# Performance work log

Measured on AMD Instinct MI355X. Metric: run time of the kernel, lower is better.

## Reference

```python
import jax, jax.numpy as jnp
import numpy as np

# ---- static dims ----
B, L, V = 8, 512, 100000
E, NERD, COREFD = 100, 20, 20          # word / ner / coref embedding dims
H, DIS, REL, HT = 128, 20, 97, 512     # hidden, dis embed, relations, n_pairs
W, N, R, C = 512, 32, 8, 256           # DNC word len, cells, read heads, ctrl hidden
IN_SIZE = E + NERD + COREFD            # 140 == H + 12 (required by final_layer)
DNC_OUT = H + 12                        # 140
CTRL_IN = IN_SIZE + R * W               # 4236
MASK_MIN, EPS, CLIP = 0.1, 1e-6, 20.0
# interface vector layout: read keys, read strengths, write key, write strength,
# erase, write vec, free gates, alloc gate, write gate, read modes,
# write mask, read masks, fwd sharpness, bwd sharpness
XI_SIZES = [R*W, R, W, 1, W, W, R, 1, 1, 3*R, W, R*W, R, R]
XI = sum(XI_SIZES)


def setup_inputs():
    key = jax.random.key(0)
    ks = iter(jax.random.split(key, 40))
    def nrm(shape, s=0.02):
        return (jax.random.normal(next(ks), shape) * s).astype(jnp.float32)
    def ri(shape, hi):
        return jax.random.randint(next(ks), shape, 0, hi)
    return dict(
        context_idxs=ri((B, L), V),
        pos=ri((B, L), L),
        context_ner=ri((B, L), 7),
        context_char_idxs=ri((B, L, 16), 262),
        context_lens=jnp.full((B,), L, dtype=jnp.int32),
        h_mapping=jax.random.uniform(next(ks), (B, HT, L), jnp.float32) / L,
        t_mapping=jax.random.uniform(next(ks), (B, HT, L), jnp.float32) / L,
        relation_mask=jnp.ones((B, HT), jnp.float32),
        dis_h_2_t=ri((B, HT), 20),
        dis_t_2_h=ri((B, HT), 20),
        word_emb=nrm((V, E), 0.1),
        entity_emb=nrm((L, COREFD), 0.1),
        ner_emb=nrm((7, NERD), 0.1),
        dis_emb=nrm((20, DIS), 0.1),
        Wih0=nrm((CTRL_IN, 4*C)), Whh0=nrm((C, 4*C)), b0=jnp.zeros((4*C,), jnp.float32),
        Wih1=nrm((C, 4*C)), Whh1=nrm((C, 4*C)), b1=jnp.zeros((4*C,), jnp.float32),
        Wih2=nrm((C, 4*C)), Whh2=nrm((C, 4*C)), b2=jnp.zeros((4*C,), jnp.float32),
        W_xi=nrm((C, XI)), b_xi=jnp.zeros((XI,), jnp.float32),
        W_out=nrm((C + R*W, DNC_OUT)), b_out=jnp.zeros((DNC_OUT,), jnp.float32),
        W_final=nrm((DNC_OUT, 2*H)), b_final=jnp.zeros((2*H,), jnp.float32),
        W_re=nrm((2*H, H)), b_re=jnp.zeros((H,), jnp.float32),
        W_bili=nrm((REL, H+DIS, H+DIS)), b_bili=jnp.zeros((REL,), jnp.float32),
    )


def _lstm(x, h, c, Wih, Whh, b):
    z = x @ Wih + h @ Whh + b
    i, f, g, o = jnp.split(z, 4, axis=-1)
    c = jax.nn.sigmoid(f) * c + jax.nn.sigmoid(i) * jnp.tanh(g)
    h = jax.nn.sigmoid(o) * jnp.tanh(c)
    return h, c


def _content(M, key_, beta, mask):
    # M [B,N,W]; key_, mask [B,h,W]; beta [B,h] -> weights [B,h,N]
    k = key_ * mask
    Mm = M[:, None] * mask[:, :, None]                 # [B,h,N,W]
    dot = jnp.einsum('bhw,bhnw->bhn', k, Mm)
    kn = jnp.linalg.norm(k, axis=-1)[..., None]
    Mn = jnp.linalg.norm(Mm, axis=-1)
    cos = dot / (kn * Mn + EPS)
    return jax.nn.softmax(beta[..., None] * cos, axis=-1)


def _sharpen(w, s):
    w = (w + EPS) ** s[..., None]
    return w / w.sum(-1, keepdims=True)


def _dnc(x, params):
    (Wih0, Whh0, b0, Wih1, Whh1, b1, Wih2, Whh2, b2, W_xi, b_xi, W_out, b_out) = params
    Bs = x.shape[0]
    eye = jnp.eye(N, dtype=x.dtype)
    splits = np.cumsum(XI_SIZES)[:-1]

    def step(carry, x_t):
        (h0, c0, h1, c1, h2, c2, M, u, wr, ww, p, Lnk, reads) = carry
        ci = jnp.concatenate([x_t, reads.reshape(Bs, R*W)], -1)
        h0, c0 = _lstm(ci, h0, c0, Wih0, Whh0, b0)
        h1, c1 = _lstm(h0, h1, c1, Wih1, Whh1, b1)
        h2, c2 = _lstm(h1, h2, c2, Wih2, Whh2, b2)
        h = jnp.clip(h2, -CLIP, CLIP)
        xi = h @ W_xi + b_xi
        (rk, rb, wk, wb, er, wv, fg, ga, gw, rm,
         wmask, rmask, sf, sb) = jnp.split(xi, splits, axis=-1)
        rk = rk.reshape(Bs, R, W)
        rb = 1 + jax.nn.softplus(rb)                    # [B,R]
        wk = wk.reshape(Bs, 1, W)
        wb = 1 + jax.nn.softplus(wb)                    # [B,1]
        er = jax.nn.sigmoid(er)                         # [B,W]
        fg = jax.nn.sigmoid(fg)                         # [B,R]
        ga = jax.nn.sigmoid(ga)
        gw = jax.nn.sigmoid(gw)
        pi = jax.nn.softmax(rm.reshape(Bs, R, 3), -1)
        wmask = MASK_MIN + (1 - MASK_MIN) * jax.nn.sigmoid(wmask)
        rmask = MASK_MIN + (1 - MASK_MIN) * jax.nn.sigmoid(rmask).reshape(Bs, R, W)
        sf = 1 + jax.nn.softplus(sf)
        sb = 1 + jax.nn.softplus(sb)

        # retention / usage
        psi = jnp.prod(1 - fg[:, :, None] * wr, axis=1)  # [B,N]
        u = (u + ww - u * ww) * psi
        # allocation weighting via sorted free list
        order = jnp.argsort(u, axis=-1)
        us = jnp.take_along_axis(u, order, -1)
        cp = jnp.cumprod(jnp.concatenate([jnp.ones((Bs, 1), u.dtype), us[:, :-1]], -1), -1)
        a_s = (1 - us) * cp
        a = jnp.zeros_like(u).at[jnp.arange(Bs)[:, None], order].set(a_s)
        # write addressing (masked content + allocation)
        cw = _content(M, wk, wb, wmask[:, None, :])[:, 0]
        ww = gw * (ga * a + (1 - ga) * cw)
        # de-allocate content of freed cells, then write
        M = M * psi[:, :, None]
        M = M * (1 - ww[:, :, None] * er[:, None, :]) + ww[:, :, None] * wv[:, None, :]
        # temporal link matrix (uses previous precedence p)
        Lnk = (1 - ww[:, :, None] - ww[:, None, :]) * Lnk + ww[:, :, None] * p[:, None, :]
        Lnk = Lnk * (1 - eye)
        p = (1 - ww.sum(-1, keepdims=True)) * p + ww
        # read addressing with link sharpness control
        fw = _sharpen(jnp.einsum('bij,brj->bri', Lnk, wr), sf)
        bw = _sharpen(jnp.einsum('bji,brj->bri', Lnk, wr), sb)
        cr = _content(M, rk, rb, rmask)
        wr = pi[..., 0:1] * bw + pi[..., 1:2] * cr + pi[..., 2:3] * fw
        reads = jnp.einsum('brn,bnw->brw', wr, M)
        y = jnp.concatenate([h, reads.reshape(Bs, R*W)], -1) @ W_out + b_out
        return (h0, c0, h1, c1, h2, c2, M, u, wr, ww, p, Lnk, reads), y

    z = jnp.zeros
    carry0 = (z((Bs, C)), z((Bs, C)), z((Bs, C)), z((Bs, C)), z((Bs, C)), z((Bs, C)),
              z((Bs, N, W)), z((Bs, N)), z((Bs, R, N)), z((Bs, N)), z((Bs, N)),
              z((Bs, N, N)), z((Bs, R, W)))
    _, ys = jax.lax.scan(step, carry0, x.transpose(1, 0, 2))
    return ys.transpose(1, 0, 2)  # [B,L,DNC_OUT]


def reference(context_idxs, pos, context_ner, context_char_idxs, context_lens,
              h_mapping, t_mapping, relation_mask, dis_h_2_t, dis_t_2_h,
              word_emb, entity_emb, ner_emb, dis_emb,
              Wih0, Whh0, b0, Wih1, Whh1, b1, Wih2, Whh2, b2,
              W_xi, b_xi, W_out, b_out, W_final, b_final, W_re, b_re,
              W_bili, b_bili):
    sent = jnp.concatenate([word_emb[context_idxs], entity_emb[pos],
                            ner_emb[context_ner]], -1)      # [B,L,140]
    dnc_params = (Wih0, Whh0, b0, Wih1, Whh1, b1, Wih2, Whh2, b2,
                  W_xi, b_xi, W_out, b_out)
    out = _dnc(sent, dnc_params)                             # [B,L,140]
    out = out @ W_final + b_final                            # LockedDropout: identity (eval)
    ctx = jax.nn.relu(out @ W_re + b_re)                     # [B,L,H]
    s0 = jnp.einsum('bpl,blh->bph', h_mapping, ctx)
    t0 = jnp.einsum('bpl,blh->bph', t_mapping, ctx)
    s_rep = jnp.concatenate([s0, dis_emb[dis_h_2_t]], -1)    # [B,P,148]
    t_rep = jnp.concatenate([t0, dis_emb[dis_t_2_h]], -1)
    return jnp.einsum('bpi,kij,bpj->bpk', s_rep, W_bili, t_rep) + b_bili
```

## Files before the change

### kernel.cpp

```cpp
#include <hip/hip_runtime.h>
#include <math.h>

#define B8      8
#define LSEQ    512
#define NWG     256
#define TPB     512
#define RELK    97
#define BI      148
#define FSTR    16
#define LDSF    39040
#define LDSB    (LDSF*4)

__device__ __forceinline__ float sigf(float x){
  return (x >= 0.f) ? 1.f/(1.f + expf(-x)) : expf(x)/(1.f + expf(x));
}
__device__ __forceinline__ float spf(float x){
  return (x > 0.f) ? x + log1pf(expf(-x)) : log1pf(expf(x));
}

__device__ __forceinline__ float agld(const float* p){
  return __hip_atomic_load(p, __ATOMIC_RELAXED, __HIP_MEMORY_SCOPE_AGENT);
}
__device__ __forceinline__ void agst(float* p, float v){
  __hip_atomic_store(p, v, __ATOMIC_RELAXED, __HIP_MEMORY_SCOPE_AGENT);
}

__global__ __launch_bounds__(256)
void k_sent(const int* __restrict__ cidx, const int* __restrict__ pos,
            const int* __restrict__ ner, const float* __restrict__ wemb,
            const float* __restrict__ eemb, const float* __restrict__ nemb,
            float* __restrict__ sent)
{
  int flat = blockIdx.x*256 + threadIdx.x;
  if (flat >= B8*LSEQ*140) return;
  int d = flat % 140; int bl = flat / 140;
  float v;
  if (d < 100)      v = wemb[(size_t)cidx[bl]*100 + d];
  else if (d < 120) v = eemb[(size_t)pos[bl]*20 + (d-100)];
  else              v = nemb[(size_t)ner[bl]*20 + (d-120)];
  sent[flat] = v;
}

__global__ __launch_bounds__(256)
void k_tr(const float* __restrict__ A, const float* __restrict__ Bsrc,
          int N, int K1a, int K1b, int K2, long long total, float* __restrict__ T)
{
  long long i = (long long)blockIdx.x*256 + threadIdx.x;
  if (i >= total) return;
  int k = (int)(i % K2);
  long long c = i / K2;
  float v = 0.f;
  if (k < K1a)            v = A[(size_t)k*N + c];
  else if (k < K1a+K1b)   v = Bsrc[(size_t)(k-K1a)*N + c];
  T[i] = v;
}

__device__ __forceinline__ void gbar(int* flags, int* genrep, int seq){
  __syncthreads();
  const int tid = threadIdx.x;
  const int bid = blockIdx.x;
  if (tid == 0){
    asm volatile("s_waitcnt vmcnt(0)" ::: "memory");
    __hip_atomic_store(&flags[bid*FSTR], seq, __ATOMIC_RELAXED, __HIP_MEMORY_SCOPE_AGENT);
  }
  if (bid == 0){
    if (tid < NWG){
      while (__hip_atomic_load(&flags[tid*FSTR], __ATOMIC_RELAXED, __HIP_MEMORY_SCOPE_AGENT) < seq)
        __builtin_amdgcn_s_sleep(2);
    }
    __syncthreads();
    if (tid < 32)
      __hip_atomic_store(&genrep[tid*FSTR], seq, __ATOMIC_RELAXED, __HIP_MEMORY_SCOPE_AGENT);
  } else if (tid == 0){
    while (__hip_atomic_load(&genrep[(bid & 31)*FSTR], __ATOMIC_RELAXED, __HIP_MEMORY_SCOPE_AGENT) < seq)
      __builtin_amdgcn_s_sleep(2);
  }
  __syncthreads();
}

__device__ void mem_phase(float* lds, const float* __restrict__ xi,
                          float* __restrict__ M, float* u_g, float* ww_g,
                          float* p_g, float* wr_g, float* L_g, float* rout)
{
  const int tid = threadIdx.x;
  float* mL  = lds;
  float* mwr = lds+1024;
  float* mwrn= lds+1280;
  float* mcr = lds+1536;
  float* mfw = lds+1792;
  float* mbw = lds+2048;
  float* PSI = lds+2304;
  float* UU  = lds+2336;
  float* US  = lds+2368;
  float* AA  = lds+2400;
  float* CW  = lds+2432;
  float* WWN = lds+2464;
  float* WWO = lds+2496;
  float* PP  = lds+2528;
  int*   mord= (int*)(lds+2560);
  float* mh  = lds+2592;
  float* mpi = lds+2656;
  float* msc = lds+2688;
  float* q1  = lds+2752;
  float* q2  = lds+3264;

  if (tid < 8){
    mh[tid]    = 1.f + spf(agld(&xi[4096+tid]));
    mh[8+tid]  = 1.f + spf(agld(&xi[10283+tid]));
    mh[16+tid] = 1.f + spf(agld(&xi[10291+tid]));
    mh[24+tid] = sigf(agld(&xi[5641+tid]));
    float e0=agld(&xi[5651+3*tid]), e1=agld(&xi[5652+3*tid]), e2=agld(&xi[5653+3*tid]);
    float mx=fmaxf(e0,fmaxf(e1,e2));
    float x0=expf(e0-mx), x1=expf(e1-mx), x2=expf(e2-mx);
    float inv=1.f/(x0+x1+x2);
    mpi[tid*3]=x0*inv; mpi[tid*3+1]=x1*inv; mpi[tid*3+2]=x2*inv;
  }
  if (tid==0){ msc[0]=1.f+spf(agld(&xi[4616])); msc[1]=sigf(agld(&xi[5649])); msc[2]=sigf(agld(&xi[5650])); }
  if (tid<32){ UU[tid]=u_g[tid]; WWO[tid]=ww_g[tid]; PP[tid]=p_g[tid]; }
  if (tid<256) mwr[tid]=wr_g[tid];
  mL[tid]=L_g[tid]; mL[tid+512]=L_g[tid+512];
  { float wm = 0.1f+0.9f*sigf(agld(&xi[5675+tid])); q1[tid]=agld(&xi[4104+tid])*wm; q2[tid]=wm; }
  __syncthreads();

  if (tid<32){
    float psi=1.f;
    #pragma unroll
    for (int r=0;r<8;r++) psi *= (1.f - mh[24+r]*mwr[r*32+tid]);
    PSI[tid]=psi;
    float uo=UU[tid], wo=WWO[tid];
    UU[tid]=(uo+wo-uo*wo)*psi;
  }
  __syncthreads();
  if (tid<32){
    float un=UU[tid]; int rank=0;
    for (int m=0;m<32;m++){ float um=UU[m]; rank += (um<un)||(um==un && m<tid); }
    mord[rank]=tid;
  }
// ... 62 lines not shown
    __syncthreads();
    if (tid==0){ float qq=0.f; for(int i=0;i<8;i++) qq+=msc[8+i]; msc[32]=sqrtf(qq); }
    __syncthreads();
    { int n=tid>>4, wsub=tid&15;
      float d=0.f,q=0.f;
      for (int i=0;i<32;i++){ int w=wsub+16*i; float m=M[(size_t)n*512+w]; float t2=m*q2[w]; d+=q1[w]*t2; q+=t2*t2; }
      for (int o=8;o;o>>=1){ d+=__shfl_down(d,o,16); q+=__shfl_down(q,o,16); }
      if (wsub==0){ float cs=d/(msc[32]*sqrtf(q)+1e-6f); mcr[r*32+n]=mh[r]*cs; } }
    __syncthreads();
  }
  if (tid<8){ int r=tid; float mx=-1e30f;
    for (int n=0;n<32;n++) mx=fmaxf(mx,mcr[r*32+n]);
    float sm=0.f;
    for (int n=0;n<32;n++){ float e=expf(mcr[r*32+n]-mx); mcr[r*32+n]=e; sm+=e; }
    float inv=1.f/sm;
    for (int n=0;n<32;n++) mcr[r*32+n]*=inv; }
  __syncthreads();
  if (tid<256){ int r=tid>>5, n=tid&31;
    float v=mpi[r*3]*mbw[r*32+n]+mpi[r*3+1]*mcr[r*32+n]+mpi[r*3+2]*mfw[r*32+n];
    mwrn[tid]=v; wr_g[tid]=v; }
  __syncthreads();
  { int r=tid>>6, wsub=tid&63;
    for (int i2=0;i2<8;i2++){ int w=wsub+64*i2;
      float accv=0.f;
      for (int n=0;n<32;n++) accv+=mwrn[r*32+n]*M[(size_t)n*512+w];
      agst(&rout[r*512+w], accv); } }
  if (tid<32){ u_g[tid]=UU[tid]; ww_g[tid]=WWN[tid]; p_g[tid]=PP[tid]; }
  L_g[tid]=mL[tid]; L_g[tid+512]=mL[tid+512];
}

__global__ __launch_bounds__(TPB, 1)
void dnc_persist(
  const float* __restrict__ sent,
  const float* __restrict__ WAg, const float* __restrict__ b0,
  const float* __restrict__ W1g, const float* __restrict__ b1,
  const float* __restrict__ W2g, const float* __restrict__ b2,
  const float* __restrict__ WXIg,const float* __restrict__ bxi,
  const float* __restrict__ WY,  const float* __restrict__ bout,
  float* __restrict__ Hh, float* __restrict__ yh,
  float* __restrict__ reads2,
  float* __restrict__ h0g, float* __restrict__ h1g, float* __restrict__ h2g,
  float* __restrict__ c0g, float* __restrict__ c1g, float* __restrict__ c2g,
  float* __restrict__ z0g, float* __restrict__ z1g, float* __restrict__ z2g,
  float* __restrict__ xig,
  float* __restrict__ Mb, float* __restrict__ ug, float* __restrict__ wwg,
  float* __restrict__ pg, float* __restrict__ wrg, float* __restrict__ Lg,
  int* flags, int* genrep)
{
  extern __shared__ float lds[];
  float* sA   = lds;
  float* sRed = lds + 4160;
  float* wA   = lds + 4224;
  float* w1l  = lds + 22656;
  float* w2l  = lds + 24704;
  float* wxl  = lds + 26752;
  const int wg  = blockIdx.x;
  const int tid = threadIdx.x;
  const int cq = tid >> 7, kq = tid & 127;
  const int xc = tid >> 6, xk = tid & 63;
  int seq = 0;

  for (int f=tid; f<18432; f+=TPB) wA[f]  = WAg[(size_t)wg*18432 + f];
  for (int f=tid; f<2048;  f+=TPB) w1l[f] = W1g[(size_t)wg*2048  + f];
  for (int f=tid; f<2048;  f+=TPB) w2l[f] = W2g[(size_t)wg*2048  + f];
  for (int f=tid; f<12288; f+=TPB){
    int cl = f>>8, k = f&255; int col = wg*48 + cl;
    wxl[f] = (col < 10299) ? WXIg[(size_t)col*256 + k] : 0.f;
  }
  const bool isy = (wg >= 8 && wg < 148);
  const float* wcolY = WY + (size_t)(isy ? (wg-8) : 0)*4352;
  __syncthreads();

  #pragma unroll 1
  for (int t=0; t<LSEQ; t++){
    const int rp = t&1, wp = rp^1, pprev = (t+1)&1;
    const float* readsPrev = reads2 + (size_t)pprev*32768;

    {
      const float* h0p = h0g + pprev*2048;
      float acc[8] = {0,0,0,0,0,0,0,0};
      float av[8];
      #pragma unroll
      for (int s=0;s<8;s++){
        int kg = tid;
        av[s] = (kg<140) ? sent[((size_t)s*512 + t)*140 + kg]
                         : agld(&readsPrev[s*4096 + kg - 140]);
      }
      #pragma unroll 1
      for (int ch=0; ch<9; ch++){
        __syncthreads();
        #pragma unroll
        for (int s=0;s<8;s++) sA[s*520 + tid] = av[s];
        __syncthreads();
        if (ch < 8){
          int kg = (ch+1)*512 + tid;
          #pragma unroll
          for (int s=0;s<8;s++){
            float v;
            if (kg < 140)       v = sent[((size_t)s*512 + t)*140 + kg];
            else if (kg < 4236) v = agld(&readsPrev[s*4096 + kg - 140]);
            else if (kg < 4492) v = agld(&h0p[s*256 + (kg-4236)]);
            else                v = 0.f;
            av[s]=v;
          }
        }
        float4 wv = *reinterpret_cast<const float4*>(&wA[cq*4608 + ch*512 + (kq<<2)]);
        #pragma unroll
        for (int s=0;s<8;s++){
          float4 a = *reinterpret_cast<const float4*>(&sA[s*520 + (kq<<2)]);
          acc[s] += a.x*wv.x + a.y*wv.y + a.z*wv.z + a.w*wv.w;
        }
      }
      #pragma unroll
      for (int o=32;o;o>>=1)
        #pragma unroll
        for (int s=0;s<8;s++) acc[s]+=__shfl_down(acc[s],o,64);
      if ((tid&63)==0){ int wv2=tid>>6;
        #pragma unroll
        for (int s=0;s<8;s++) sRed[wv2*8+s]=acc[s]; }
      __syncthreads();
      if (tid<32){ int c=tid>>3, s=tid&7;
        agst(&z0g[s*1024 + wg*4 + c], sRed[c*16+s] + sRed[c*16+8+s] + b0[wg*4+c]); }
    }
    gbar(flags,genrep,++seq);

    {
      float4 w1v = *reinterpret_cast<const float4*>(&w1l[cq*512 + (kq<<2)]);
      if (tid<256){
        int j=tid;
        #pragma unroll
        for (int s=0;s<8;s++){
          float zi=agld(&z0g[s*1024+j]), zf=agld(&z0g[s*1024+256+j]);
          float zg=agld(&z0g[s*1024+512+j]), zo=agld(&z0g[s*1024+768+j]);
          float cold=agld(&c0g[rp*2048+s*256+j]);
          float cn=sigf(zf)*cold+sigf(zi)*tanhf(zg);
          float h=sigf(zo)*tanhf(cn);
          sA[s*520+j]=h;
          if (wg==8){ agst(&c0g[wp*2048+s*256+j],cn); agst(&h0g[rp*2048+s*256+j],h); }
        }
      } else {
        int j=tid-256;
        const float* h1p = h1g + pprev*2048;
        #pragma unroll
        for (int s=0;s<8;s++) sA[s*520+256+j]=agld(&h1p[s*256+j]);
      }
      __syncthreads();
      float acc[8]={0,0,0,0,0,0,0,0};
      #pragma unroll
      for (int s=0;s<8;s++){
        float4 a=*reinterpret_cast<const float4*>(&sA[s*520+(kq<<2)]);
        acc[s]+=a.x*w1v.x+a.y*w1v.y+a.z*w1v.z+a.w*w1v.w;
      }
      #pragma unroll
      for (int o=32;o;o>>=1)
        #pragma unroll
        for (int s=0;s<8;s++) acc[s]+=__shfl_down(acc[s],o,64);
      if ((tid&63)==0){ int wv2=tid>>6;
        #pragma unroll
        for (int s=0;s<8;s++) sRed[wv2*8+s]=acc[s]; }
      __syncthreads();
      if (tid<32){ int c=tid>>3, s=tid&7;
        agst(&z1g[s*1024 + wg*4 + c], sRed[c*16+s] + sRed[c*16+8+s] + b1[wg*4+c]); }
    }
    gbar(flags,genrep,++seq);

    {
      float4 w2v = *reinterpret_cast<const float4*>(&w2l[cq*512 + (kq<<2)]);
      if (tid<256){
        int j=tid;
        #pragma unroll
        for (int s=0;s<8;s++){
          float zi=agld(&z1g[s*1024+j]), zf=agld(&z1g[s*1024+256+j]);
          float zg=agld(&z1g[s*1024+512+j]), zo=agld(&z1g[s*1024+768+j]);
          float cold=agld(&c1g[rp*2048+s*256+j]);
          float cn=sigf(zf)*cold+sigf(zi)*tanhf(zg);
          float h=sigf(zo)*tanhf(cn);
          sA[s*520+j]=h;
          if (wg==8){ agst(&c1g[wp*2048+s*256+j],cn); agst(&h1g[rp*2048+s*256+j],h); }
        }
      } else {
        int j=tid-256;
        const float* h2p = h2g + pprev*2048;
        #pragma unroll
        for (int s=0;s<8;s++) sA[s*520+256+j]=agld(&h2p[s*256+j]);
      }
      __syncthreads();
      float acc[8]={0,0,0,0,0,0,0,0};
      #pragma unroll
      for (int s=0;s<8;s++){
        float4 a=*reinterpret_cast<const float4*>(&sA[s*520+(kq<<2)]);
        acc[s]+=a.x*w2v.x+a.y*w2v.y+a.z*w2v.z+a.w*w2v.w;
      }
      #pragma unroll
      for (int o=32;o;o>>=1)
        #pragma unroll
        for (int s=0;s<8;s++) acc[s]+=__shfl_down(acc[s],o,64);
      if ((tid&63)==0){ int wv2=tid>>6;
        #pragma unroll
        for (int s=0;s<8;s++) sRed[wv2*8+s]=acc[s]; }
      __syncthreads();
      if (tid<32){ int c=tid>>3, s=tid&7;
        agst(&z2g[s*1024 + wg*4 + c], sRed[c*16+s] + sRed[c*16+8+s] + b2[wg*4+c]); }
    }
    gbar(flags,genrep,++seq);

    {
      if (tid<256){
        int j=tid;
        #pragma unroll
        for (int s=0;s<8;s++){
          float zi=agld(&z2g[s*1024+j]), zf=agld(&z2g[s*1024+256+j]);
          float zg=agld(&z2g[s*1024+512+j]), zo=agld(&z2g[s*1024+768+j]);
          float cold=agld(&c2g[rp*2048+s*256+j]);
          float cn=sigf(zf)*cold+sigf(zi)*tanhf(zg);
          float h2=sigf(zo)*tanhf(cn);
          float hc=fminf(fmaxf(h2,-20.f),20.f);
          sA[s*520+j]=hc;
          if (wg==8){ agst(&c2g[wp*2048+s*256+j],cn); agst(&h2g[rp*2048+s*256+j],h2);
                      agst(&Hh[((size_t)t*8+s)*256+j],hc); }
        }
      }
      __syncthreads();
      float accx[6][8];
      #pragma unroll
      for (int cc=0;cc<6;cc++)
        #pragma unroll
        for (int s=0;s<8;s++) accx[cc][s]=0.f;
      #pragma unroll
      for (int s=0;s<8;s++){
        float4 a = *reinterpret_cast<const float4*>(&sA[s*520 + (xk<<2)]);
        #pragma unroll
        for (int cc=0;cc<6;cc++){
          float4 wv = *reinterpret_cast<const float4*>(&wxl[(xc*6+cc)*256 + (xk<<2)]);
          accx[cc][s] += a.x*wv.x + a.y*wv.y + a.z*wv.z + a.w*wv.w;
        }
      }
      #pragma unroll
      for (int o=32;o;o>>=1)
        #pragma unroll
        for (int cc=0;cc<6;cc++)
          #pragma unroll
          for (int s=0;s<8;s++) accx[cc][s]+=__shfl_down(accx[cc][s],o,64);
      if ((tid&63)==0){
        #pragma unroll
        for (int cc=0;cc<6;cc++){
          int col = wg*48 + xc*6 + cc;
          if (col < 10299){
            #pragma unroll
            for (int s=0;s<8;s++) agst(&xig[(size_t)s*10299+col], accx[cc][s]+bxi[col]);
          }
        }
      }
    }
    gbar(flags,genrep,++seq);

    if (wg < 8){
      mem_phase(lds, xig + (size_t)wg*10299, Mb + (size_t)wg*16384,
                ug+wg*32, wwg+wg*32, pg+wg*32, wrg+wg*256, Lg+wg*1024,
                reads2 + (size_t)rp*32768 + wg*4096);
    } else if (isy && t > 0){
      int ty = t-1;
      const float* rdp = reads2 + (size_t)(ty&1)*32768;
      float wy[9];
      #pragma unroll
      for (int ch=0;ch<9;ch++){ int k=ch*512+tid; wy[ch]=(k<4352)? wcolY[k] : 0.f; }
      float acy[8]={0,0,0,0,0,0,0,0};
      #pragma unroll
      for (int ch=0;ch<9;ch++){
        int kg=ch*512+tid;
        #pragma unroll
        for (int s=0;s<8;s++){
          float a;
          if (kg<256)       a=agld(&Hh[((size_t)ty*8+s)*256+kg]);
          else if (kg<4352) a=agld(&rdp[s*4096+kg-256]);
          else              a=0.f;
          acy[s]+=a*wy[ch];
        }
      }
      #pragma unroll
      for (int o=32;o;o>>=1)
        #pragma unroll
        for (int s=0;s<8;s++) acy[s]+=__shfl_down(acy[s],o,64);
      if ((tid&63)==0){ int wv2=tid>>6;
        #pragma unroll
        for (int s=0;s<8;s++) sRed[wv2*8+s]=acy[s]; }
      __syncthreads();
      if (tid<8){ float v=0.f;
        #pragma unroll
        for (int w=0;w<8;w++) v+=sRed[w*8+tid];
        yh[((size_t)tid*512+ty)*140+(wg-8)]=v+bout[wg-8]; }
    }
    gbar(flags,genrep,++seq);
  }

  if (isy){
    int ty = 511;
    const float* rdp = reads2 + (size_t)(ty&1)*32768;
    float wy[9];
    #pragma unroll
    for (int ch=0;ch<9;ch++){ int k=ch*512+tid; wy[ch]=(k<4352)? wcolY[k] : 0.f; }
    float acy[8]={0,0,0,0,0,0,0,0};
    #pragma unroll
    for (int ch=0;ch<9;ch++){
      int kg=ch*512+tid;
      #pragma unroll
      for (int s=0;s<8;s++){
        float a;
        if (kg<256)       a=agld(&Hh[((size_t)ty*8+s)*256+kg]);
        else if (kg<4352) a=agld(&rdp[s*4096+kg-256]);
        else              a=0.f;
        acy[s]+=a*wy[ch];
      }
    }
    #pragma unroll
    for (int o=32;o;o>>=1)
      #pragma unroll
      for (int s=0;s<8;s++) acy[s]+=__shfl_down(acy[s],o,64);
    if ((tid&63)==0){ int wv2=tid>>6;
      #pragma unroll
      for (int s=0;s<8;s++) sRed[wv2*8+s]=acy[s]; }
    __syncthreads();
    if (tid<8){ float v=0.f;
      #pragma unroll
      for (int w=0;w<8;w++) v+=sRed[w*8+tid];
      yh[((size_t)tid*512+ty)*140+(wg-8)]=v+bout[wg-8]; }
  }
}

__global__ __launch_bounds__(256)
void gemm16(int M, int N, int K,
            const float* __restrict__ A, long long sAb, int lda,
            const float* __restrict__ Bm, long long sBb, int ldb,
            float* __restrict__ C, long long sCb, int ldc,
            const float* __restrict__ bias, int relu)
{
  __shared__ float sAh[16*512];
  const int tid = threadIdx.x;
  const float* Ab = A + (size_t)blockIdx.y*sAb;
  const float* Bb = Bm + (size_t)blockIdx.y*sBb;
  float* Cb = C + (size_t)blockIdx.y*sCb;
  const int m0 = blockIdx.x*16;
  const int tot = 16*K;
  for (int f = tid; f < tot; f += 256) sAh[f] = Ab[(size_t)m0*lda + f];
  __syncthreads();
  int c = (tid & 63)*4; int rg = tid >> 6;
  if (c >= N) return;
  float acc[4][4] = {};
  for (int k=0;k<K;k++){
    float4 bv = *reinterpret_cast<const float4*>(Bb + (size_t)k*ldb + c);
    #pragma unroll
    for (int rr=0;rr<4;rr++){
      float a = sAh[(rg*4+rr)*K + k];
      acc[rr][0] += a*bv.x; acc[rr][1] += a*bv.y; acc[rr][2] += a*bv.z; acc[rr][3] += a*bv.w;
    }
  }
  for (int rr=0;rr<4;rr++){
    int m = m0 + rg*4 + rr;
    #pragma unroll
// ... 75 lines not shown
  const int*   ctx_idx = (const int*)  d_in[0];
  const int*   pos     = (const int*)  d_in[1];
  const int*   nerI    = (const int*)  d_in[2];
  const float* h_map   = (const float*)d_in[5];
  const float* t_map   = (const float*)d_in[6];
  const int*   dht     = (const int*)  d_in[8];
  const int*   dth     = (const int*)  d_in[9];
  const float* wemb    = (const float*)d_in[10];
  const float* eemb    = (const float*)d_in[11];
  const float* nemb    = (const float*)d_in[12];
  const float* demb    = (const float*)d_in[13];
  const float* Wih0    = (const float*)d_in[14];
  const float* Whh0    = (const float*)d_in[15];
  const float* b0      = (const float*)d_in[16];
  const float* Wih1    = (const float*)d_in[17];
  const float* Whh1    = (const float*)d_in[18];
  const float* b1      = (const float*)d_in[19];
  const float* Wih2    = (const float*)d_in[20];
  const float* Whh2    = (const float*)d_in[21];
  const float* b2      = (const float*)d_in[22];
  const float* Wxi     = (const float*)d_in[23];
  const float* bxi     = (const float*)d_in[24];
  const float* Wout    = (const float*)d_in[25];
  const float* bout    = (const float*)d_in[26];
  const float* Wfin    = (const float*)d_in[27];
  const float* bfin    = (const float*)d_in[28];
  const float* Wre     = (const float*)d_in[29];
  const float* bre     = (const float*)d_in[30];
  const float* Wbili   = (const float*)d_in[31];
  const float* bbili   = (const float*)d_in[32];

  float* ws    = (float*)d_ws;
  float* sent  = ws;
  float* Hh    = sent + 573440;
  float* yh    = Hh + 1048576;
  float* s0b   = yh + 573440;
  float* t0b   = s0b + 524288;
  float* reads2= t0b + 524288;
  float* h0g   = reads2 + 65536;
  float* h1g   = h0g + 4096;
  float* h2g   = h1g + 4096;
  float* c0g   = h2g + 4096;
  float* c1g   = c0g + 4096;
  float* c2g   = c1g + 4096;
  float* z0g   = c2g + 4096;
  float* z1g   = z0g + 8192;
  float* z2g   = z1g + 8192;
  float* xig   = z2g + 8192;
  float* Mb    = xig + 82392;
  float* ug    = Mb + 131072;
  float* wwg   = ug + 256;
  float* pg    = wwg + 256;
  float* wrg   = pg + 256;
  float* Lg    = wrg + 2048;
  float* barf  = Lg + 8192;
  float* WA_T  = barf + 4608;
  float* W1T   = WA_T + 4718592;
  float* W2T   = W1T + 524288;
  float* WXIT  = W2T + 524288;
  float* WYT   = WXIT + 2636544;
  float* o256  = Hh;
  float* ctxb  = sent;
  int* flags  = (int*)barf;
  int* genrep = flags + 256*FSTR;

  size_t stateFloats = (size_t)(WA_T - reads2);
  hipMemsetAsync(reads2, 0, stateFloats*sizeof(float), stream);

  hipLaunchKernelGGL(k_tr, dim3(18432), dim3(256), 0, stream,
                     Wih0, Whh0, 1024, 4236, 256, 4608, (long long)4718592, WA_T);
  hipLaunchKernelGGL(k_tr, dim3(2048), dim3(256), 0, stream,
                     Wih1, Whh1, 1024, 256, 256, 512, (long long)524288, W1T);
  hipLaunchKernelGGL(k_tr, dim3(2048), dim3(256), 0, stream,
                     Wih2, Whh2, 1024, 256, 256, 512, (long long)524288, W2T);
  hipLaunchKernelGGL(k_tr, dim3(10299), dim3(256), 0, stream,
                     Wxi, Wxi, 10299, 256, 0, 256, (long long)2636544, WXIT);
  hipLaunchKernelGGL(k_tr, dim3(2380), dim3(256), 0, stream,
                     Wout, Wout, 140, 4352, 0, 4352, (long long)609280, WYT);

  hipLaunchKernelGGL(k_sent, dim3((573440+255)/256), dim3(256), 0, stream,
                     ctx_idx, pos, nerI, wemb, eemb, nemb, sent);

  hipFuncSetAttribute(reinterpret_cast<const void*>(dnc_persist),
                      hipFuncAttributeMaxDynamicSharedMemorySize, LDSB);

  hipLaunchKernelGGL(dnc_persist, dim3(NWG), dim3(TPB), LDSB, stream,
                     sent, WA_T, b0, W1T, b1, W2T, b2, WXIT, bxi, WYT, bout,
                     Hh, yh, reads2,
                     h0g, h1g, h2g, c0g, c1g, c2g, z0g, z1g, z2g, xig,
                     Mb, ug, wwg, pg, wrg, Lg, flags, genrep);

  hipLaunchKernelGGL(gemm16, dim3(256,1), dim3(256), 0, stream,
                     4096, 256, 140, yh, (long long)0, 140, Wfin, (long long)0, 256,
                     o256, (long long)0, 256, bfin, 0);
  hipLaunchKernelGGL(gemm16, dim3(256,1), dim3(256), 0, stream,
                     4096, 128, 256, o256, (long long)0, 256, Wre, (long long)0, 128,
                     ctxb, (long long)0, 128, bre, 1);
  hipLaunchKernelGGL(gemm16, dim3(32,8), dim3(256), 0, stream,
                     512, 128, 512, h_map, (long long)(512*512), 512,
                     ctxb, (long long)(512*128), 128,
                     s0b, (long long)(512*128), 128, (const float*)nullptr, 0);
  hipLaunchKernelGGL(gemm16, dim3(32,8), dim3(256), 0, stream,
                     512, 128, 512, t_map, (long long)(512*512), 512,
                     ctxb, (long long)(512*128), 128,
                     t0b, (long long)(512*128), 128, (const float*)nullptr, 0);
  hipLaunchKernelGGL(bilin, dim3(128,2), dim3(256), 0, stream,
                     s0b, t0b, demb, dht, dth, Wbili, bbili, (float*)d_out);
}
```

Baseline: 88.91 ms.

## Re-partition persistent DNC LSTM work as 2D K-split tiles with separate gate reduction

Each workgroup of the persistent kernel now holds a column-by-K tile of each LSTM weight matrix and of the output projection in LDS, loaded directly from the original weights. Host-side transposes are removed, leaving only the xi transpose. Every workgroup writes partial sums, and 64 workgroups reduce them and apply the gate nonlinearities. The output projection is split across all workgroups and reduced with a wave shuffle, which replaces the full 4352-long per-column dot product that read weights from global memory. The price is extra global barriers per timestep (a reduce phase after each layer and a final step), more partial-sum traffic, and a per-workgroup release flag with shorter sleeps in the barrier.

```diff
diff --git a/kernel.cpp b/kernel.cpp
--- a/kernel.cpp
+++ b/kernel.cpp
@@ -8,7 +8,14 @@
 #define RELK    97
 #define BI      148
 #define FSTR    16
-#define LDSF    39040
+
+#define oWA     0
+#define oW1     18432
+#define oW2     20480
+#define oWX     22528
+#define oWY     34816
+#define oST     37196
+#define LDSF    40948
 #define LDSB    (LDSF*4)
 
 __device__ __forceinline__ float sigf(float x){
@@ -17,7 +24,6 @@
 __device__ __forceinline__ float spf(float x){
   return (x > 0.f) ? x + log1pf(expf(-x)) : log1pf(expf(x));
 }
-
 __device__ __forceinline__ float agld(const float* p){
   return __hip_atomic_load(p, __ATOMIC_RELAXED, __HIP_MEMORY_SCOPE_AGENT);
 }
@@ -66,14 +72,14 @@
   if (bid == 0){
     if (tid < NWG){
       while (__hip_atomic_load(&flags[tid*FSTR], __ATOMIC_RELAXED, __HIP_MEMORY_SCOPE_AGENT) < seq)
-        __builtin_amdgcn_s_sleep(2);
+        __builtin_amdgcn_s_sleep(1);
     }
     __syncthreads();
-    if (tid < 32)
+    if (tid < NWG)
       __hip_atomic_store(&genrep[tid*FSTR], seq, __ATOMIC_RELAXED, __HIP_MEMORY_SCOPE_AGENT);
   } else if (tid == 0){
-    while (__hip_atomic_load(&genrep[(bid & 31)*FSTR], __ATOMIC_RELAXED, __HIP_MEMORY_SCOPE_AGENT) < seq)
-      __builtin_amdgcn_s_sleep(2);
+    while (__hip_atomic_load(&genrep[bid*FSTR], __ATOMIC_RELAXED, __HIP_MEMORY_SCOPE_AGENT) < seq)
+      __builtin_amdgcn_s_sleep(1);
   }
   __syncthreads();
 }
@@ -99,10 +105,10 @@
   float* PP  = lds+2528;
   int*   mord= (int*)(lds+2560);
   float* mh  = lds+2592;
-  float* mpi = lds+2656;
-  float* msc = lds+2688;
-  float* q1  = lds+2752;
-  float* q2  = lds+3264;
+  float* mpi = lds+2624;
+  float* msc = lds+2648;
+  float* q1  = lds+2688;
+  float* q2  = lds+3200;
 
   if (tid < 8){
     mh[tid]    = 1.f + spf(agld(&xi[4096+tid]));
@@ -231,194 +237,204 @@
 __global__ __launch_bounds__(TPB, 1)
 void dnc_persist(
   const float* __restrict__ sent,
-  const float* __restrict__ WAg, const float* __restrict__ b0,
-  const float* __restrict__ W1g, const float* __restrict__ b1,
-  const float* __restrict__ W2g, const float* __restrict__ b2,
-  const float* __restrict__ WXIg,const float* __restrict__ bxi,
-  const float* __restrict__ WY,  const float* __restrict__ bout,
-  float* __restrict__ Hh, float* __restrict__ yh,
-  float* __restrict__ reads2,
-  float* __restrict__ h0g, float* __restrict__ h1g, float* __restrict__ h2g,
-  float* __restrict__ c0g, float* __restrict__ c1g, float* __restrict__ c2g,
-  float* __restrict__ z0g, float* __restrict__ z1g, float* __restrict__ z2g,
-  float* __restrict__ xig,
+  const float* __restrict__ Wih0, const float* __restrict__ Whh0, const float* __restrict__ b0,
+  const float* __restrict__ Wih1, const float* __restrict__ Whh1, const float* __restrict__ b1,
+  const float* __restrict__ Wih2, const float* __restrict__ Whh2, const float* __restrict__ b2,
+  const float* __restrict__ WXIT, const float* __restrict__ bxi,
+  const float* __restrict__ Wout, const float* __restrict__ bout,
+  float* __restrict__ yh,
+  float* __restrict__ reads,
+  float* __restrict__ h0, float* __restrict__ h1,
+  float* __restrict__ h2u, float* __restrict__ h2c,
+  float* __restrict__ c0p, float* __restrict__ c1p, float* __restrict__ c2p,
+  float* __restrict__ zp0, float* __restrict__ zp1, float* __restrict__ zp2,
+  float* __restrict__ yp, float* __restrict__ xig,
   float* __restrict__ Mb, float* __restrict__ ug, float* __restrict__ wwg,
   float* __restrict__ pg, float* __restrict__ wrg, float* __restrict__ Lg,
   int* flags, int* genrep)
 {
   extern __shared__ float lds[];
-  float* sA   = lds;
-  float* sRed = lds + 4160;
-  float* wA   = lds + 4224;
-  float* w1l  = lds + 22656;
-  float* w2l  = lds + 24704;
-  float* wxl  = lds + 26752;
   const int wg  = blockIdx.x;
   const int tid = threadIdx.x;
-  const int cq = tid >> 7, kq = tid & 127;
-  const int xc = tid >> 6, xk = tid & 63;
+  const int cg  = wg >> 4, kg  = wg & 15;
+  const int cgB = wg >> 3, kgB = wg & 7;
+  const int ycg = wg >> 6, ykg = wg & 63;
+  const int xc  = tid >> 6, xk = tid & 63;
+  float* stg = lds + oST;
   int seq = 0;
 
-  for (int f=tid; f<18432; f+=TPB) wA[f]  = WAg[(size_t)wg*18432 + f];
-  for (int f=tid; f<2048;  f+=TPB) w1l[f] = W1g[(size_t)wg*2048  + f];
-  for (int f=tid; f<2048;  f+=TPB) w2l[f] = W2g[(size_t)wg*2048  + f];
+  for (int f=tid; f<18432; f+=TPB){
+    int kk=f>>6, cc=f&63;
+    int gk=kg*288+kk, gc=cg*64+cc;
+    float v=0.f;
+    if (gk<4236) v=Wih0[(size_t)gk*1024+gc];
+    else if (gk<4492) v=Whh0[(size_t)(gk-4236)*1024+gc];
+    lds[oWA+f]=v;
+  }
+  for (int f=tid; f<2048; f+=TPB){
+    int kk=f>>5, cc=f&31;
+    int gk=kgB*64+kk, gc=cgB*32+cc;
+    lds[oW1+f] = (gk<256)? Wih1[(size_t)gk*1024+gc] : Whh1[(size_t)(gk-256)*1024+gc];
+  }
+  for (int f=tid; f<2048; f+=TPB){
+    int kk=f>>5, cc=f&31;
+    int gk=kgB*64+kk, gc=cgB*32+cc;
+    lds[oW2+f] = (gk<256)? Wih2[(size_t)gk*1024+gc] : Whh2[(size_t)(gk-256)*1024+gc];
+  }
   for (int f=tid; f<12288; f+=TPB){
-    int cl = f>>8, k = f&255; int col = wg*48 + cl;
-    wxl[f] = (col < 10299) ? WXIg[(size_t)col*256 + k] : 0.f;
-  }
-  const bool isy = (wg >= 8 && wg < 148);
-  const float* wcolY = WY + (size_t)(isy ? (wg-8) : 0)*4352;
+    int cl=f>>8, k=f&255; int col=wg*48+cl;
+    lds[oWX+f] = (col<10299)? WXIT[(size_t)col*256+k] : 0.f;
+  }
+  for (int f=tid; f<2380; f+=TPB){
+    int kk=f/35, cc=f%35;
+    int gk=ykg*68+kk, gc=ycg*35+cc;
+    lds[oWY+f] = Wout[(size_t)gk*140+gc];
+  }
   __syncthreads();
 
   #pragma unroll 1
   for (int t=0; t<LSEQ; t++){
-    const int rp = t&1, wp = rp^1, pprev = (t+1)&1;
-    const float* readsPrev = reads2 + (size_t)pprev*32768;
-
     {
-      const float* h0p = h0g + pprev*2048;
-      float acc[8] = {0,0,0,0,0,0,0,0};
-      float av[8];
-      #pragma unroll
-      for (int s=0;s<8;s++){
-        int kg = tid;
-        av[s] = (kg<140) ? sent[((size_t)s*512 + t)*140 + kg]
-                         : agld(&readsPrev[s*4096 + kg - 140]);
-      }
-      #pragma unroll 1
-      for (int ch=0; ch<9; ch++){
-        __syncthreads();
+      float* sAct = stg;
+      float* sActY= stg+2304;
+      for (int f=tid; f<2304; f+=TPB){
+        int s=f/288, kk=f%288; int g=kg*288+kk;
+        float v;
+        if (g<140)       v = sent[((size_t)s*512+t)*140+g];
+        else if (g<4236) v = agld(&reads[s*4096+g-140]);
+        else if (g<4492) v = agld(&h0[s*256+(g-4236)]);
+        else             v = 0.f;
+        sAct[f]=v;
+      }
+      if (t>0) for (int f=tid; f<544; f+=TPB){
+        int s=f/68, kk=f%68; int gy=ykg*68+kk;
+        sActY[f] = (gy<256)? agld(&h2c[s*256+gy]) : agld(&reads[s*4096+gy-256]);
+      }
+      __syncthreads();
+      { int cc=tid&63, s=tid>>6;
+        const float* wAl = lds+oWA;
+        const float* ac  = sAct + s*288;
+        float acc=0.f;
+        #pragma unroll 8
+        for (int kk=0; kk<288; kk++) acc += wAl[kk*64+cc]*ac[kk];
+        agst(&zp0[(size_t)(kg*8+s)*1024 + cg*64+cc], acc); }
+      if (t>0 && tid<280){ int s=tid/35, cc=tid%35;
+        const float* wYl = lds+oWY;
+        const float* ac  = sActY + s*68;
+        float acc=0.f;
+        #pragma unroll 4
+        for (int kk=0; kk<68; kk++) acc += wYl[kk*35+cc]*ac[kk];
+        agst(&yp[(size_t)(ykg*8+s)*144 + ycg*35+cc], acc); }
+    }
+    gbar(flags,genrep,++seq);
+
+    if (wg < 64){
+      int s = wg>>3, part = wg&7;
+      float* sP = stg;
+      { int j32=tid&31, q=(tid>>5)&3, kp=tid>>7;
+        int col = q*256 + part*32 + j32;
+        float v=0.f;
+        for (int k2=kp*4; k2<kp*4+4; k2++) v += agld(&zp0[(size_t)(k2*8+s)*1024+col]);
+        sP[kp*128 + q*32 + j32] = v; }
+      __syncthreads();
+      if (tid<32){
+        int j = part*32 + tid;
+        float zq[4];
         #pragma unroll
-        for (int s=0;s<8;s++) sA[s*520 + tid] = av[s];
-        __syncthreads();
-        if (ch < 8){
-          int kg = (ch+1)*512 + tid;
-          #pragma unroll
-          for (int s=0;s<8;s++){
-            float v;
-            if (kg < 140)       v = sent[((size_t)s*512 + t)*140 + kg];
-            else if (kg < 4236) v = agld(&readsPrev[s*4096 + kg - 140]);
-            else if (kg < 4492) v = agld(&h0p[s*256 + (kg-4236)]);
-            else                v = 0.f;
-            av[s]=v;
-          }
-        }
-        float4 wv = *reinterpret_cast<const float4*>(&wA[cq*4608 + ch*512 + (kq<<2)]);
+        for (int q=0;q<4;q++){ float v=0.f;
+          for (int k2=0;k2<4;k2++) v += sP[k2*128+q*32+tid];
+          zq[q]=v + b0[q*256+j]; }
+        float cold=c0p[s*256+j];
+        float cn=sigf(zq[1])*cold + sigf(zq[0])*tanhf(zq[2]);
+        float h=sigf(zq[3])*tanhf(cn);
+        c0p[s*256+j]=cn;
+        agst(&h0[s*256+j], h);
+      }
+    }
+    gbar(flags,genrep,++seq);
+
+    {
+      float* sAct = stg;
+      for (int f=tid; f<512; f+=TPB){ int s=f>>6, kk=f&63; int g=kgB*64+kk;
+        sAct[f] = (g<256)? agld(&h0[s*256+g]) : agld(&h1[s*256+g-256]); }
+      __syncthreads();
+      if (tid<256){ int cc=tid&31, s=tid>>5;
+        const float* w1l = lds+oW1;
+        const float* ac  = sAct + s*64;
+        float acc=0.f;
+        #pragma unroll 8
+        for (int kk=0; kk<64; kk++) acc += w1l[kk*32+cc]*ac[kk];
+        agst(&zp1[(size_t)(kgB*8+s)*1024 + cgB*32+cc], acc); }
+    }
+    gbar(flags,genrep,++seq);
+
+    if (wg < 64){
+      int s = wg>>3, part = wg&7;
+      float* sP = stg;
+      if (tid<256){ int j32=tid&31, q=(tid>>5)&3, kp=tid>>7;
+        int col = q*256 + part*32 + j32;
+        float v=0.f;
+        for (int k2=kp*4; k2<kp*4+4; k2++) v += agld(&zp1[(size_t)(k2*8+s)*1024+col]);
+        sP[kp*128 + q*32 + j32] = v; }
+      __syncthreads();
+      if (tid<32){
+        int j = part*32 + tid;
+        float zq[4];
         #pragma unroll
-        for (int s=0;s<8;s++){
-          float4 a = *reinterpret_cast<const float4*>(&sA[s*520 + (kq<<2)]);
-          acc[s] += a.x*wv.x + a.y*wv.y + a.z*wv.z + a.w*wv.w;
-        }
-      }
-      #pragma unroll
-      for (int o=32;o;o>>=1)
+        for (int q=0;q<4;q++) zq[q]=sP[q*32+tid]+sP[128+q*32+tid]+b1[q*256+j];
+        float cold=c1p[s*256+j];
+        float cn=sigf(zq[1])*cold + sigf(zq[0])*tanhf(zq[2]);
+        float h=sigf(zq[3])*tanhf(cn);
+        c1p[s*256+j]=cn;
+        agst(&h1[s*256+j], h);
+      }
+    }
+    gbar(flags,genrep,++seq);
+
+    {
+      float* sAct = stg;
+      for (int f=tid; f<512; f+=TPB){ int s=f>>6, kk=f&63; int g=kgB*64+kk;
+        sAct[f] = (g<256)? agld(&h1[s*256+g]) : agld(&h2u[s*256+g-256]); }
+      __syncthreads();
+      if (tid<256){ int cc=tid&31, s=tid>>5;
+        const float* w2l = lds+oW2;
+        const float* ac  = sAct + s*64;
+        float acc=0.f;
+        #pragma unroll 8
+        for (int kk=0; kk<64; kk++) acc += w2l[kk*32+cc]*ac[kk];
+        agst(&zp2[(size_t)(kgB*8+s)*1024 + cgB*32+cc], acc); }
+    }
+    gbar(flags,genrep,++seq);
+
+    if (wg < 64){
+      int s = wg>>3, part = wg&7;
+      float* sP = stg;
+      if (tid<256){ int j32=tid&31, q=(tid>>5)&3, kp=tid>>7;
+        int col = q*256 + part*32 + j32;
+        float v=0.f;
+        for (int k2=kp*4; k2<kp*4+4; k2++) v += agld(&zp2[(size_t)(k2*8+s)*1024+col]);
+        sP[kp*128 + q*32 + j32] = v; }
+      __syncthreads();
+      if (tid<32){
+        int j = part*32 + tid;
+        float zq[4];
         #pragma unroll
-        for (int s=0;s<8;s++) acc[s]+=__shfl_down(acc[s],o,64);
-      if ((tid&63)==0){ int wv2=tid>>6;
-        #pragma unroll
-        for (int s=0;s<8;s++) sRed[wv2*8+s]=acc[s]; }
-      __syncthreads();
-      if (tid<32){ int c=tid>>3, s=tid&7;
-        agst(&z0g[s*1024 + wg*4 + c], sRed[c*16+s] + sRed[c*16+8+s] + b0[wg*4+c]); }
+        for (int q=0;q<4;q++) zq[q]=sP[q*32+tid]+sP[128+q*32+tid]+b2[q*256+j];
+        float cold=c2p[s*256+j];
+        float cn=sigf(zq[1])*cold + sigf(zq[0])*tanhf(zq[2]);
+        float h2=sigf(zq[3])*tanhf(cn);
+        float hc=fminf(fmaxf(h2,-20.f),20.f);
+        c2p[s*256+j]=cn;
+        agst(&h2u[s*256+j], h2);
+        agst(&h2c[s*256+j], hc);
+      }
     }
     gbar(flags,genrep,++seq);
 
     {
-      float4 w1v = *reinterpret_cast<const float4*>(&w1l[cq*512 + (kq<<2)]);
-      if (tid<256){
-        int j=tid;
-        #pragma unroll
-        for (int s=0;s<8;s++){
-          float zi=agld(&z0g[s*1024+j]), zf=agld(&z0g[s*1024+256+j]);
-          float zg=agld(&z0g[s*1024+512+j]), zo=agld(&z0g[s*1024+768+j]);
-          float cold=agld(&c0g[rp*2048+s*256+j]);
-          float cn=sigf(zf)*cold+sigf(zi)*tanhf(zg);
-          float h=sigf(zo)*tanhf(cn);
-          sA[s*520+j]=h;
-          if (wg==8){ agst(&c0g[wp*2048+s*256+j],cn); agst(&h0g[rp*2048+s*256+j],h); }
-        }
-      } else {
-        int j=tid-256;
-        const float* h1p = h1g + pprev*2048;
-        #pragma unroll
-        for (int s=0;s<8;s++) sA[s*520+256+j]=agld(&h1p[s*256+j]);
-      }
-      __syncthreads();
-      float acc[8]={0,0,0,0,0,0,0,0};
-      #pragma unroll
-      for (int s=0;s<8;s++){
-        float4 a=*reinterpret_cast<const float4*>(&sA[s*520+(kq<<2)]);
-        acc[s]+=a.x*w1v.x+a.y*w1v.y+a.z*w1v.z+a.w*w1v.w;
-      }
-      #pragma unroll
-      for (int o=32;o;o>>=1)
-        #pragma unroll
-        for (int s=0;s<8;s++) acc[s]+=__shfl_down(acc[s],o,64);
-      if ((tid&63)==0){ int wv2=tid>>6;
-        #pragma unroll
-        for (int s=0;s<8;s++) sRed[wv2*8+s]=acc[s]; }
-      __syncthreads();
-      if (tid<32){ int c=tid>>3, s=tid&7;
-        agst(&z1g[s*1024 + wg*4 + c], sRed[c*16+s] + sRed[c*16+8+s] + b1[wg*4+c]); }
-    }
-    gbar(flags,genrep,++seq);
-
-    {
-      float4 w2v = *reinterpret_cast<const float4*>(&w2l[cq*512 + (kq<<2)]);
-      if (tid<256){
-        int j=tid;
-        #pragma unroll
-        for (int s=0;s<8;s++){
-          float zi=agld(&z1g[s*1024+j]), zf=agld(&z1g[s*1024+256+j]);
-          float zg=agld(&z1g[s*1024+512+j]), zo=agld(&z1g[s*1024+768+j]);
-          float cold=agld(&c1g[rp*2048+s*256+j]);
-          float cn=sigf(zf)*cold+sigf(zi)*tanhf(zg);
-          float h=sigf(zo)*tanhf(cn);
-          sA[s*520+j]=h;
-          if (wg==8){ agst(&c1g[wp*2048+s*256+j],cn); agst(&h1g[rp*2048+s*256+j],h); }
-        }
-      } else {
-        int j=tid-256;
-        const float* h2p = h2g + pprev*2048;
-        #pragma unroll
-        for (int s=0;s<8;s++) sA[s*520+256+j]=agld(&h2p[s*256+j]);
-      }
-      __syncthreads();
-      float acc[8]={0,0,0,0,0,0,0,0};
-      #pragma unroll
-      for (int s=0;s<8;s++){
-        float4 a=*reinterpret_cast<const float4*>(&sA[s*520+(kq<<2)]);
-        acc[s]+=a.x*w2v.x+a.y*w2v.y+a.z*w2v.z+a.w*w2v.w;
-      }
-      #pragma unroll
-      for (int o=32;o;o>>=1)
-        #pragma unroll
-        for (int s=0;s<8;s++) acc[s]+=__shfl_down(acc[s],o,64);
-      if ((tid&63)==0){ int wv2=tid>>6;
-        #pragma unroll
-        for (int s=0;s<8;s++) sRed[wv2*8+s]=acc[s]; }
-      __syncthreads();
-      if (tid<32){ int c=tid>>3, s=tid&7;
-        agst(&z2g[s*1024 + wg*4 + c], sRed[c*16+s] + sRed[c*16+8+s] + b2[wg*4+c]); }
-    }
-    gbar(flags,genrep,++seq);
-
-    {
-      if (tid<256){
-        int j=tid;
-        #pragma unroll
-        for (int s=0;s<8;s++){
-          float zi=agld(&z2g[s*1024+j]), zf=agld(&z2g[s*1024+256+j]);
-          float zg=agld(&z2g[s*1024+512+j]), zo=agld(&z2g[s*1024+768+j]);
-          float cold=agld(&c2g[rp*2048+s*256+j]);
-          float cn=sigf(zf)*cold+sigf(zi)*tanhf(zg);
-          float h2=sigf(zo)*tanhf(cn);
-          float hc=fminf(fmaxf(h2,-20.f),20.f);
-          sA[s*520+j]=hc;
-          if (wg==8){ agst(&c2g[wp*2048+s*256+j],cn); agst(&h2g[rp*2048+s*256+j],h2);
-                      agst(&Hh[((size_t)t*8+s)*256+j],hc); }
-        }
-      }
+      float* sA2 = stg;
+      for (int f=tid; f<2048; f+=TPB){ int s=f>>8, j=f&255;
+        sA2[s*260+j] = agld(&h2c[s*256+j]); }
       __syncthreads();
       float accx[6][8];
       #pragma unroll
@@ -427,10 +443,10 @@
         for (int s=0;s<8;s++) accx[cc][s]=0.f;
       #pragma unroll
       for (int s=0;s<8;s++){
-        float4 a = *reinterpret_cast<const float4*>(&sA[s*520 + (xk<<2)]);
+        float4 a = *reinterpret_cast<const float4*>(&sA2[s*260 + (xk<<2)]);
         #pragma unroll
         for (int cc=0;cc<6;cc++){
-          float4 wv = *reinterpret_cast<const float4*>(&wxl[(xc*6+cc)*256 + (xk<<2)]);
+          float4 wv = *reinterpret_cast<const float4*>(&lds[oWX + (xc*6+cc)*256 + (xk<<2)]);
           accx[cc][s] += a.x*wv.x + a.y*wv.y + a.z*wv.z + a.w*wv.w;
         }
       }
@@ -454,75 +470,42 @@
     gbar(flags,genrep,++seq);
 
     if (wg < 8){
-      mem_phase(lds, xig + (size_t)wg*10299, Mb + (size_t)wg*16384,
+      mem_phase(stg, xig + (size_t)wg*10299, Mb + (size_t)wg*16384,
                 ug+wg*32, wwg+wg*32, pg+wg*32, wrg+wg*256, Lg+wg*1024,
-                reads2 + (size_t)rp*32768 + wg*4096);
-    } else if (isy && t > 0){
-      int ty = t-1;
-      const float* rdp = reads2 + (size_t)(ty&1)*32768;
-      float wy[9];
+                reads + wg*4096);
+    } else if (wg < 148 && t > 0){
+      int ty = t-1, j = wg-8;
+      int s = tid>>6, kg2 = tid&63;
+      float v = agld(&yp[(size_t)(kg2*8+s)*144 + j]);
       #pragma unroll
-      for (int ch=0;ch<9;ch++){ int k=ch*512+tid; wy[ch]=(k<4352)? wcolY[k] : 0.f; }
-      float acy[8]={0,0,0,0,0,0,0,0};
-      #pragma unroll
-      for (int ch=0;ch<9;ch++){
-        int kg=ch*512+tid;
-        #pragma unroll
-        for (int s=0;s<8;s++){
-          float a;
-          if (kg<256)       a=agld(&Hh[((size_t)ty*8+s)*256+kg]);
-          else if (kg<4352) a=agld(&rdp[s*4096+kg-256]);
-          else              a=0.f;
-          acy[s]+=a*wy[ch];
-        }
-      }
-      #pragma unroll
-      for (int o=32;o;o>>=1)
-        #pragma unroll
-        for (int s=0;s<8;s++) acy[s]+=__shfl_down(acy[s],o,64);
-      if ((tid&63)==0){ int wv2=tid>>6;
-        #pragma unroll
-        for (int s=0;s<8;s++) sRed[wv2*8+s]=acy[s]; }
-      __syncthreads();
-      if (tid<8){ float v=0.f;
-        #pragma unroll
-        for (int w=0;w<8;w++) v+=sRed[w*8+tid];
-        yh[((size_t)tid*512+ty)*140+(wg-8)]=v+bout[wg-8]; }
+      for (int o=32;o;o>>=1) v += __shfl_down(v,o,64);
+      if (kg2==0) yh[((size_t)s*512+ty)*140+j] = v + bout[j];
     }
     gbar(flags,genrep,++seq);
   }
 
-  if (isy){
-    int ty = 511;
-    const float* rdp = reads2 + (size_t)(ty&1)*32768;
-    float wy[9];
+  {
+    float* sActY = stg;
+    for (int f=tid; f<544; f+=TPB){
+      int s=f/68, kk=f%68; int gy=ykg*68+kk;
+      sActY[f] = (gy<256)? agld(&h2c[s*256+gy]) : agld(&reads[s*4096+gy-256]);
+    }
+    __syncthreads();
+    if (tid<280){ int s=tid/35, cc=tid%35;
+      const float* wYl = lds+oWY;
+      const float* ac  = sActY + s*68;
+      float acc=0.f;
+      for (int kk=0; kk<68; kk++) acc += wYl[kk*35+cc]*ac[kk];
+      agst(&yp[(size_t)(ykg*8+s)*144 + ycg*35+cc], acc); }
+  }
+  gbar(flags,genrep,++seq);
+  if (wg>=8 && wg<148){
+    int j = wg-8;
+    int s = tid>>6, kg2 = tid&63;
+    float v = agld(&yp[(size_t)(kg2*8+s)*144 + j]);
     #pragma unroll
-    for (int ch=0;ch<9;ch++){ int k=ch*512+tid; wy[ch]=(k<4352)? wcolY[k] : 0.f; }
-    float acy[8]={0,0,0,0,0,0,0,0};
-    #pragma unroll
-    for (int ch=0;ch<9;ch++){
-      int kg=ch*512+tid;
-      #pragma unroll
-      for (int s=0;s<8;s++){
-        float a;
-        if (kg<256)       a=agld(&Hh[((size_t)ty*8+s)*256+kg]);
-        else if (kg<4352) a=agld(&rdp[s*4096+kg-256]);
-        else              a=0.f;
-        acy[s]+=a*wy[ch];
-      }
-    }
-    #pragma unroll
-    for (int o=32;o;o>>=1)
-      #pragma unroll
-      for (int s=0;s<8;s++) acy[s]+=__shfl_down(acy[s],o,64);
-    if ((tid&63)==0){ int wv2=tid>>6;
-      #pragma unroll
-      for (int s=0;s<8;s++) sRed[wv2*8+s]=acy[s]; }
-    __syncthreads();
-    if (tid<8){ float v=0.f;
-      #pragma unroll
-      for (int w=0;w<8;w++) v+=sRed[w*8+tid];
-      yh[((size_t)tid*512+ty)*140+(wg-8)]=v+bout[wg-8]; }
+    for (int o=32;o;o>>=1) v += __shfl_down(v,o,64);
+    if (kg2==0) yh[((size_t)s*512+511)*140+j] = v + bout[j];
   }
 }
 
@@ -664,52 +647,41 @@
 
   float* ws    = (float*)d_ws;
   float* sent  = ws;
-  float* Hh    = sent + 573440;
-  float* yh    = Hh + 1048576;
-  float* s0b   = yh + 573440;
+  float* yh    = sent + 573440;
+  float* o256  = yh + 573440;
+  float* s0b   = o256 + 1048576;
   float* t0b   = s0b + 524288;
-  float* reads2= t0b + 524288;
-  float* h0g   = reads2 + 65536;
-  float* h1g   = h0g + 4096;
-  float* h2g   = h1g + 4096;
-  float* c0g   = h2g + 4096;
-  float* c1g   = c0g + 4096;
-  float* c2g   = c1g + 4096;
-  float* z0g   = c2g + 4096;
-  float* z1g   = z0g + 8192;
-  float* z2g   = z1g + 8192;
-  float* xig   = z2g + 8192;
-  float* Mb    = xig + 82392;
-  float* ug    = Mb + 131072;
-  float* wwg   = ug + 256;
-  float* pg    = wwg + 256;
-  float* wrg   = pg + 256;
-  float* Lg    = wrg + 2048;
-  float* barf  = Lg + 8192;
-  float* WA_T  = barf + 4608;
-  float* W1T   = WA_T + 4718592;
-  float* W2T   = W1T + 524288;
-  float* WXIT  = W2T + 524288;
-  float* WYT   = WXIT + 2636544;
-  float* o256  = Hh;
-  float* ctxb  = sent;
+  float* SB    = t0b + 524288;
+  float* reads = SB + 0;
+  float* h0    = SB + 32768;
+  float* h1    = SB + 34816;
+  float* h2u   = SB + 36864;
+  float* h2c   = SB + 38912;
+  float* c0p   = SB + 40960;
+  float* c1p   = SB + 43008;
+  float* c2p   = SB + 45056;
+  float* zp0   = SB + 47104;
+  float* zp1   = SB + 178176;
+  float* zp2   = SB + 243712;
+  float* yp    = SB + 309248;
+  float* xig   = SB + 382976;
+  float* Mb    = SB + 465368;
+  float* ug    = SB + 596440;
+  float* wwg   = SB + 596696;
+  float* pg    = SB + 596952;
+  float* wrg   = SB + 597208;
+  float* Lg    = SB + 599256;
+  float* barf  = SB + 607448;
+  float* SEnd  = SB + 615640;
+  float* WXIT  = SEnd;
+  float* ctxb  = yh;
   int* flags  = (int*)barf;
   int* genrep = flags + 256*FSTR;
 
-  size_t stateFloats = (size_t)(WA_T - reads2);
-  hipMemsetAsync(reads2, 0, stateFloats*sizeof(float), stream);
-
-  hipLaunchKernelGGL(k_tr, dim3(18432), dim3(256), 0, stream,
-                     Wih0, Whh0, 1024, 4236, 256, 4608, (long long)4718592, WA_T);
-  hipLaunchKernelGGL(k_tr, dim3(2048), dim3(256), 0, stream,
-                     Wih1, Whh1, 1024, 256, 256, 512, (long long)524288, W1T);
-  hipLaunchKernelGGL(k_tr, dim3(2048), dim3(256), 0, stream,
-                     Wih2, Whh2, 1024, 256, 256, 512, (long long)524288, W2T);
+  hipMemsetAsync(SB, 0, (size_t)615640*sizeof(float), stream);
+
   hipLaunchKernelGGL(k_tr, dim3(10299), dim3(256), 0, stream,
                      Wxi, Wxi, 10299, 256, 0, 256, (long long)2636544, WXIT);
-  hipLaunchKernelGGL(k_tr, dim3(2380), dim3(256), 0, stream,
-                     Wout, Wout, 140, 4352, 0, 4352, (long long)609280, WYT);
-
   hipLaunchKernelGGL(k_sent, dim3((573440+255)/256), dim3(256), 0, stream,
                      ctx_idx, pos, nerI, wemb, eemb, nemb, sent);
 
@@ -717,9 +689,10 @@
                       hipFuncAttributeMaxDynamicSharedMemorySize, LDSB);
 
   hipLaunchKernelGGL(dnc_persist, dim3(NWG), dim3(TPB), LDSB, stream,
-                     sent, WA_T, b0, W1T, b1, W2T, b2, WXIT, bxi, WYT, bout,
-                     Hh, yh, reads2,
-                     h0g, h1g, h2g, c0g, c1g, c2g, z0g, z1g, z2g, xig,
+                     sent, Wih0, Whh0, b0, Wih1, Whh1, b1, Wih2, Whh2, b2,
+                     WXIT, bxi, Wout, bout, yh, reads,
+                     h0, h1, h2u, h2c, c0p, c1p, c2p,
+                     zp0, zp1, zp2, yp, xig,
                      Mb, ug, wwg, pg, wrg, Lg, flags, genrep);
 
   hipLaunchKernelGGL(gemm16, dim3(256,1), dim3(256), 0, stream,
```

Measured after the change: 90.09 ms. Within noise of the previous version (+1.3%).
